# Kernel tuning notes

Measured on AMD Instinct MI355X. Metric: run time of the kernel, lower is better.

Reference implementation:

```python
import jax, jax.numpy as jnp
import numpy as np

N, D_IN, D_OUT = 8192, 256, 128

def setup_inputs() -> dict:
    key = jax.random.key(0)
    kx, kq, kk, kv = jax.random.split(key, 4)
    x = jax.random.normal(kx, (N, D_IN), dtype=jnp.float32)
    # original uses torch.rand (uniform [0,1)) for parameters
    weight_query = jax.random.uniform(kq, (D_IN, D_OUT), dtype=jnp.float32)
    weight_key = jax.random.uniform(kk, (D_IN, D_OUT), dtype=jnp.float32)
    weight_value = jax.random.uniform(kv, (D_IN, D_OUT), dtype=jnp.float32)
    return {"x": x, "weight_query": weight_query, "weight_key": weight_key, "weight_value": weight_value}

def reference(x, weight_query, weight_key, weight_value):
    queries = x @ weight_query            # [N, d_out]
    keys = x @ weight_key                 # [N, d_out]
    values = x @ weight_value             # [N, d_out]
    scale = 1.0 / jnp.sqrt(jnp.asarray(keys.shape[-1], dtype=keys.dtype))
    scores = (queries @ keys.T) * scale   # [N, N] — full score matrix, as in original
    weights = jax.nn.softmax(scores, axis=-1)
    return weights @ values               # [N, d_out]
```

## Files before the change

### kernel.cpp

```cpp
#include <hip/hip_runtime.h>
#include <math.h>


typedef float f32x4 __attribute__((ext_vector_type(4)));
typedef float f32x16 __attribute__((ext_vector_type(16)));
typedef __bf16 bf16x8 __attribute__((ext_vector_type(8)));
typedef unsigned short ushort_t;
typedef ushort_t us4 __attribute__((ext_vector_type(4)));
typedef unsigned u32x2 __attribute__((ext_vector_type(2)));

#define N_TOK 8192
#define NSPLIT 8
#define NSTEP 16

static __device__ __forceinline__ f32x16 mfma32(bf16x8 a, bf16x8 b, f32x16 c) {
  return __builtin_amdgcn_mfma_f32_32x32x16_bf16(a, b, c, 0, 0, 0);
}
static __device__ __forceinline__ void f2split(float f, ushort_t& hi, ushort_t& lo) {
  __bf16 h = (__bf16)f;
  float rem = f - (float)h;
  __bf16 l2 = (__bf16)rem;
  hi = __builtin_bit_cast(ushort_t, h);
  lo = __builtin_bit_cast(ushort_t, l2);
}
static __device__ __forceinline__ void gload16(const void* g, void* l) {
  __builtin_amdgcn_global_load_lds(
      (const __attribute__((address_space(1))) unsigned*)g,
      (__attribute__((address_space(3))) unsigned*)l, 16, 0, 0);
}
static __device__ __forceinline__ unsigned cvtpk(float lo, float hi) {
  unsigned w;
  asm("v_cvt_pk_bf16_f32 %0, %1, %2" : "=v"(w) : "v"(lo), "v"(hi));
  return w;
}

__global__ __launch_bounds__(256) void prep_kernel(
    const float* __restrict__ X, const float* __restrict__ Wq,
    const float* __restrict__ Wk, const float* __restrict__ Wv,
    ushort_t* __restrict__ Xh, ushort_t* __restrict__ Xl,
    ushort_t* __restrict__ WTh, ushort_t* __restrict__ WTl) {
  int gid = blockIdx.x * 256 + threadIdx.x;
  if (gid < 524288) {
    float4 v = reinterpret_cast<const float4*>(X)[gid];
    us4 h, l;
    ushort_t hh, ll;
    f2split(v.x, hh, ll); h[0] = hh; l[0] = ll;
    f2split(v.y, hh, ll); h[1] = hh; l[1] = ll;
    f2split(v.z, hh, ll); h[2] = hh; l[2] = ll;
    f2split(v.w, hh, ll); h[3] = hh; l[3] = ll;
    reinterpret_cast<us4*>(Xh)[gid] = h;
    reinterpret_cast<us4*>(Xl)[gid] = l;
  } else if (gid < 524288 + 98304) {
    int e = gid - 524288;
    int y = e >> 15, r = e & 32767;
    int k = r >> 7, c = r & 127;
    const float* W = (y == 0) ? Wq : (y == 1) ? Wk : Wv;
    ushort_t h, l;
    f2split(W[r], h, l);
    WTh[y * 32768 + c * 256 + k] = h;
    WTl[y * 32768 + c * 256 + k] = l;
  }
}

__global__ __launch_bounds__(256) void proj_kernel(
    const ushort_t* __restrict__ Xh, const ushort_t* __restrict__ Xl,
    const ushort_t* __restrict__ WTh, const ushort_t* __restrict__ WTl,
    ushort_t* __restrict__ Qh, ushort_t* __restrict__ Ql,
    ushort_t* __restrict__ Kh, ushort_t* __restrict__ Kl,
    ushort_t* __restrict__ VTh, ushort_t* __restrict__ VTl) {
  __shared__ __align__(16) char sm[49152];
  const int SXH = 0, SXL = 8192, SWH = 16384, SWL = 32768;
  int t = threadIdx.x, l = t & 63, wid = t >> 6;
  int c32 = l & 31, h = l >> 5;
  int wr = wid >> 1, wc = wid & 1;
  int t0 = blockIdx.x * 64, y = blockIdx.y;
  const ushort_t* WThy = WTh + y * 32768;
  const ushort_t* WTly = WTl + y * 32768;

  f32x16 zero = {};
  f32x16 acc[2];
  acc[0] = zero; acc[1] = zero;

  for (int sl = 0; sl < 4; ++sl) {
    int k0 = sl * 64;
    __syncthreads();
    #pragma unroll
    for (int j = 0; j < 12; ++j) {
      int id = wid * 12 + j;
      const ushort_t* src;
      char* dst;
      if (id < 16) {
        const ushort_t* base = (id < 8) ? Xh : Xl;
        int c_ = id & 7;
        int row = 8 * c_ + (l >> 3);
        int slot = l & 7;
        src = base + (size_t)(t0 + row) * 256 + k0 + ((slot ^ (row & 7)) * 8);
        dst = sm + ((id < 8) ? SXH : SXL) + c_ * 1024 + l * 16;
      } else {
        const ushort_t* base = (id < 32) ? WThy : WTly;
        int c_ = (id - 16) & 15;
        int row = 8 * c_ + (l >> 3);
        int slot = l & 7;
        src = base + (size_t)row * 256 + k0 + ((slot ^ (row & 7)) * 8);
        dst = sm + ((id < 32) ? SWH : SWL) + c_ * 1024 + l * 16;
      }
      gload16(src, dst);
    }
    asm volatile("s_waitcnt vmcnt(0)" ::: "memory");
    __syncthreads();
    #pragma unroll
    for (int ks = 0; ks < 4; ++ks) {
      int ar = 32 * wr + c32;
      int ao = ar * 128 + (((2 * ks + h) ^ (ar & 7)) * 16);
      bf16x8 ah = *(const bf16x8*)(sm + SXH + ao);
      bf16x8 axl = *(const bf16x8*)(sm + SXL + ao);
      #pragma unroll
      for (int ct = 0; ct < 2; ++ct) {
        int bc = 64 * wc + 32 * ct + c32;
        int bo = bc * 128 + (((2 * ks + h) ^ (bc & 7)) * 16);
        bf16x8 bh = *(const bf16x8*)(sm + SWH + bo);
        bf16x8 bl2 = *(const bf16x8*)(sm + SWL + bo);
        acc[ct] = mfma32(ah, bh, acc[ct]);
        acc[ct] = mfma32(ah, bl2, acc[ct]);
        acc[ct] = mfma32(axl, bh, acc[ct]);
      }
    }
  }

  const float QS = 0.12751744f;
  if (y < 2) {
    ushort_t* Hh = y ? Kh : Qh;
    ushort_t* Hl = y ? Kl : Ql;
    #pragma unroll
    for (int ct = 0; ct < 2; ++ct)
      #pragma unroll
      for (int r = 0; r < 16; ++r) {
        float v = acc[ct][r];
        if (y == 0) v *= QS;
        int rt = t0 + 32 * wr + (r & 3) + 8 * (r >> 2) + 4 * h;
        int cc = 64 * wc + 32 * ct + c32;
        ushort_t hh, ll;
        f2split(v, hh, ll);
        Hh[(size_t)rt * 128 + cc] = hh;
        Hl[(size_t)rt * 128 + cc] = ll;
      }
  } else {
    __syncthreads();
    #pragma unroll
    for (int ct = 0; ct < 2; ++ct)
      #pragma unroll
      for (int r = 0; r < 16; ++r) {
        float v = acc[ct][r];
        int rtl = 32 * wr + (r & 3) + 8 * (r >> 2) + 4 * h;
        int cc = 64 * wc + 32 * ct + c32;
        ushort_t hh, ll;
        f2split(v, hh, ll);
        *(ushort_t*)(sm + rtl * 272 + cc * 2) = hh;
        *(ushort_t*)(sm + 17408 + rtl * 272 + cc * 2) = ll;
      }
    __syncthreads();
    int cc = t >> 1, hs = t & 1;
    #pragma unroll
    for (int jj = 0; jj < 4; ++jj) {
      int r0 = hs * 32 + jj * 8;
      us4 a, b, a2, b2;
      #pragma unroll
      for (int e = 0; e < 4; ++e) {
        a[e]  = *(const ushort_t*)(sm + (r0 + e) * 272 + cc * 2);
        b[e]  = *(const ushort_t*)(sm + (r0 + 4 + e) * 272 + cc * 2);
        a2[e] = *(const ushort_t*)(sm + 17408 + (r0 + e) * 272 + cc * 2);
        b2[e] = *(const ushort_t*)(sm + 17408 + (r0 + 4 + e) * 272 + cc * 2);
      }
      *(us4*)(VTh + (size_t)cc * N_TOK + t0 + r0) = a;
      *(us4*)(VTh + (size_t)cc * N_TOK + t0 + r0 + 4) = b;
      *(us4*)(VTl + (size_t)cc * N_TOK + t0 + r0) = a2;
      *(us4*)(VTl + (size_t)cc * N_TOK + t0 + r0 + 4) = b2;
    }
  }
}

__global__ __launch_bounds__(256, 2) void attn_kernel(
    const ushort_t* __restrict__ Qh, const ushort_t* __restrict__ Ql,
    const ushort_t* __restrict__ Kh, const ushort_t* __restrict__ Kl,
    const ushort_t* __restrict__ VTh, const ushort_t* __restrict__ VTl,
    float* __restrict__ Op, float* __restrict__ mp, float* __restrict__ lp) {
  extern __shared__ __align__(16) char sm[];
  const int OKH = 0, OKL = 16384, OVH = 32768, OVL = 49152;
  int t = threadIdx.x, l = t & 63, wid = t >> 6;
  int c32 = l & 31, h = l >> 5;
  int bid = blockIdx.x;
  int split = bid & 7, qt = bid >> 3;
  int qb = qt * 128, kv0 = split * 1024;
  int q_lane = qb + wid * 32 + c32;

  bf16x8 qfh[8], qfl[8];
  #pragma unroll
  for (int ks = 0; ks < 8; ++ks) {
    qfh[ks] = *(const bf16x8*)(Qh + (size_t)q_lane * 128 + ks * 16 + h * 8);
    qfl[ks] = *(const bf16x8*)(Ql + (size_t)q_lane * 128 + ks * 16 + h * 8);
  }

  f32x16 zero = {};
  f32x16 od[4];
  #pragma unroll
  for (int dt = 0; dt < 4; ++dt) od[dt] = zero;
  float m = -INFINITY, lsum = 0.f;

  for (int s = 0; s < NSTEP; ++s) {
    int kb = kv0 + s * 64;
    __syncthreads();
    #pragma unroll
    for (int j = 0; j < 16; ++j) {
      int id = wid * 16 + j;
      const ushort_t* src;
      char* dst;
      if (id < 32) {
        const ushort_t* base = (id < 16) ? Kh : Kl;
        int c_ = id & 15;
        int row = 4 * c_ + (l >> 4);
        int slot = l & 15;
        src = base + (size_t)(kb + row) * 128 + ((slot ^ (row & 15)) * 8);
        dst = sm + ((id < 16) ? OKH : OKL) + c_ * 1024 + l * 16;
      } else {
        const ushort_t* base = (id < 48) ? VTh : VTl;
        int c_ = id & 15;
        int d = 8 * c_ + (l >> 3);
        int slot = l & 7;
        src = base + (size_t)d * N_TOK + kb + ((slot ^ (d & 7)) * 8);
        dst = sm + ((id < 48) ? OVH : OVL) + c_ * 1024 + l * 16;
      }
      gload16(src, dst);
    }
    asm volatile("s_waitcnt vmcnt(0)" ::: "memory");
    __syncthreads();

    f32x16 sc0 = zero, sc1 = zero;
    #pragma unroll
    for (int ks = 0; ks < 8; ++ks) {
      int so = ((2 * ks + h) ^ (c32 & 15)) * 16;
      bf16x8 a0h = *(const bf16x8*)(sm + OKH + c32 * 256 + so);
      bf16x8 a0l = *(const bf16x8*)(sm + OKL + c32 * 256 + so);
      bf16x8 a1h = *(const bf16x8*)(sm + OKH + 8192 + c32 * 256 + so);
      bf16x8 a1l = *(const bf16x8*)(sm + OKL + 8192 + c32 * 256 + so);
      sc0 = mfma32(a0h, qfh[ks], sc0);
      sc0 = mfma32(a0h, qfl[ks], sc0);
      sc0 = mfma32(a0l, qfh[ks], sc0);
      sc1 = mfma32(a1h, qfh[ks], sc1);
      sc1 = mfma32(a1h, qfl[ks], sc1);
      sc1 = mfma32(a1l, qfh[ks], sc1);
    }

    float pm = sc0[0];
    #pragma unroll
    for (int r = 1; r < 16; ++r) pm = fmaxf(pm, sc0[r]);
    #pragma unroll
    for (int r = 0; r < 16; ++r) pm = fmaxf(pm, sc1[r]);
    pm = fmaxf(pm, __shfl_xor(pm, 32));
    float mn = fmaxf(m, pm);
    float al = exp2f(m - mn);
    m = mn;
    float ps = 0.f;
    #pragma unroll
    for (int r = 0; r < 16; ++r) { sc0[r] = exp2f(sc0[r] - m); ps += sc0[r]; }
    #pragma unroll
    for (int r = 0; r < 16; ++r) { sc1[r] = exp2f(sc1[r] - m); ps += sc1[r]; }
    lsum = lsum * al + ps;
    #pragma unroll
    for (int dt = 0; dt < 4; ++dt) od[dt] *= al;

    bf16x8 pf[4];
    #pragma unroll
    for (int ks = 0; ks < 4; ++ks) {
      const f32x16& P = (ks < 2) ? sc0 : sc1;
      int r0 = 8 * (ks & 1);
      unsigned A0 = cvtpk(P[r0 + 0], P[r0 + 1]);
      unsigned A1 = cvtpk(P[r0 + 2], P[r0 + 3]);
      unsigned B0 = cvtpk(P[r0 + 4], P[r0 + 5]);
      unsigned B1 = cvtpk(P[r0 + 6], P[r0 + 7]);
      u32x2 s0 = __builtin_amdgcn_permlane32_swap(A0, B0, false, false);
      u32x2 s1 = __builtin_amdgcn_permlane32_swap(A1, B1, false, false);
      union { unsigned u[4]; bf16x8 v; } cvt;
      cvt.u[0] = s0[0]; cvt.u[1] = s1[0]; cvt.u[2] = s0[1]; cvt.u[3] = s1[1];
      pf[ks] = cvt.v;
    }

    #pragma unroll
    for (int ks = 0; ks < 4; ++ks) {
      #pragma unroll
      for (int dt = 0; dt < 4; ++dt) {
        int row = 32 * dt + c32;
        int so2 = row * 128 + (((2 * ks + h) ^ (c32 & 7)) * 16);
        bf16x8 vh = *(const bf16x8*)(sm + OVH + so2);
        bf16x8 vl2 = *(const bf16x8*)(sm + OVL + so2);
        od[dt] = mfma32(vh, pf[ks], od[dt]);
        od[dt] = mfma32(vl2, pf[ks], od[dt]);
      }
    }
  }

  lsum += __shfl_xor(lsum, 32);
  #pragma unroll
  for (int dt = 0; dt < 4; ++dt)
    #pragma unroll
    for (int r = 0; r < 16; ++r) {
      int d = 32 * dt + (r & 3) + 8 * (r >> 2) + 4 * h;
      Op[(size_t)(split * 128 + d) * N_TOK + q_lane] = od[dt][r];
    }
  if (h == 0) {
    mp[split * N_TOK + q_lane] = m;
    lp[split * N_TOK + q_lane] = lsum;
  }
}

__global__ __launch_bounds__(256) void merge_kernel(
    const float* __restrict__ Op, const float* __restrict__ mp,
    const float* __restrict__ lp, float* __restrict__ out) {
  __shared__ float accs[32][129];
  __shared__ float Ls[32];
  int t = threadIdx.x;
  int q0 = blockIdx.x * 32;
  int ql = t & 31, dr = t >> 5;
  float mm[NSPLIT], ll[NSPLIT];
  #pragma unroll
  for (int s2 = 0; s2 < NSPLIT; ++s2) {
    mm[s2] = mp[s2 * N_TOK + q0 + ql];
    ll[s2] = lp[s2 * N_TOK + q0 + ql];
  }
  float M = mm[0];
  #pragma unroll
  for (int s2 = 1; s2 < NSPLIT; ++s2) M = fmaxf(M, mm[s2]);
  float w[NSPLIT], L = 0.f;
  #pragma unroll
  for (int s2 = 0; s2 < NSPLIT; ++s2) { w[s2] = exp2f(mm[s2] - M); L += w[s2] * ll[s2]; }
  if (dr == 0) Ls[ql] = L;
  for (int dd = dr; dd < 128; dd += 8) {
    float a = 0.f;
    #pragma unroll
    for (int s2 = 0; s2 < NSPLIT; ++s2)
      a += w[s2] * Op[(size_t)(s2 * 128 + dd) * N_TOK + q0 + ql];
    accs[ql][dd] = a;
  }
  __syncthreads();
  int q = t >> 3, db = (t & 7) * 16;
  float inv = 1.0f / Ls[q];
  #pragma unroll
  for (int jj = 0; jj < 4; ++jj) {
    f32x4 v;
    #pragma unroll
    for (int e = 0; e < 4; ++e) v[e] = accs[q][db + jj * 4 + e] * inv;
    *reinterpret_cast<f32x4*>(out + (size_t)(q0 + q) * 128 + db + jj * 4) = v;
  }
}

extern "C" void kernel_launch(void* const* d_in, const int* in_sizes, int n_in,
                              void* d_out, int out_size, void* d_ws, size_t ws_size,
                              hipStream_t stream) {
  (void)in_sizes; (void)n_in; (void)out_size; (void)ws_size;
  const float* X  = (const float*)d_in[0];
  const float* Wq = (const float*)d_in[1];
  const float* Wk = (const float*)d_in[2];
  const float* Wv = (const float*)d_in[3];
  float* out = (float*)d_out;
  char* ws = (char*)d_ws;

  const size_t MB = 1048576;
  ushort_t* Qh  = (ushort_t*)(ws + 0 * MB);
  ushort_t* Ql  = (ushort_t*)(ws + 2 * MB);
  ushort_t* Kh  = (ushort_t*)(ws + 4 * MB);
  ushort_t* Kl  = (ushort_t*)(ws + 6 * MB);
  ushort_t* VTh = (ushort_t*)(ws + 8 * MB);
  ushort_t* VTl = (ushort_t*)(ws + 10 * MB);
  float* mpp = (float*)(ws + 12 * MB);
  float* lpp = (float*)(ws + 12 * MB + 262144);
  float* Op  = (float*)(ws + 12 * MB + 524288);
  ushort_t* Xh  = (ushort_t*)(ws + 12 * MB + 524288);
  ushort_t* Xl  = (ushort_t*)(ws + 16 * MB + 524288);
  ushort_t* WTh = (ushort_t*)(ws + 20 * MB + 524288);
  ushort_t* WTl = (ushort_t*)(ws + 20 * MB + 524288 + 196608);

  (void)hipFuncSetAttribute((const void*)attn_kernel,
                            hipFuncAttributeMaxDynamicSharedMemorySize, 65536);

  prep_kernel<<<2432, 256, 0, stream>>>(X, Wq, Wk, Wv, Xh, Xl, WTh, WTl);
  proj_kernel<<<dim3(128, 3), 256, 0, stream>>>(Xh, Xl, WTh, WTl,
                                                Qh, Ql, Kh, Kl, VTh, VTl);
  attn_kernel<<<512, 256, 65536, stream>>>(Qh, Ql, Kh, Kl, VTh, VTl, Op, mpp, lpp);
  merge_kernel<<<256, 256, 0, stream>>>(Op, mpp, lpp, out);
}
```

Baseline: 168.4 us.

## Double-buffer 32-token KV tiles with async prefetch and lazy softmax rescale

Restructures the attention inner loop to process 32-key tiles instead of 64, double-buffered in LDS so the next tile's K/V global-to-LDS loads overlap the current tile's MFMA and softmax work. Each wave now issues a fixed set of precomputed load offsets for one of the four streams (Kh, Kl, VTh, VTl). It also adds a lazy max rescale that only updates m and rescales the accumulators when the new max exceeds the old by more than 8, and sets wave priority around the MFMA blocks. The trade-offs are twice as many loop iterations with an extra barrier each, plus a redundant wraparound prefetch on the last step.

```diff
diff --git a/kernel.cpp b/kernel.cpp
--- a/kernel.cpp
+++ b/kernel.cpp
@@ -11,7 +11,8 @@
 
 #define N_TOK 8192
 #define NSPLIT 8
-#define NSTEP 16
+#define KVB 32
+#define NSTEP2 32
 
 static __device__ __forceinline__ f32x16 mfma32(bf16x8 a, bf16x8 b, f32x16 c) {
   return __builtin_amdgcn_mfma_f32_32x32x16_bf16(a, b, c, 0, 0, 0);
@@ -185,7 +186,6 @@
     const ushort_t* __restrict__ VTh, const ushort_t* __restrict__ VTl,
     float* __restrict__ Op, float* __restrict__ mp, float* __restrict__ lp) {
   extern __shared__ __align__(16) char sm[];
-  const int OKH = 0, OKL = 16384, OVH = 32768, OVL = 49152;
   int t = threadIdx.x, l = t & 63, wid = t >> 6;
   int c32 = l & 31, h = l >> 5;
   int bid = blockIdx.x;
@@ -200,83 +200,92 @@
     qfl[ks] = *(const bf16x8*)(Ql + (size_t)q_lane * 128 + ks * 16 + h * 8);
   }
 
+  const ushort_t* gbase;
+  int stepstride;
+  int offs[8];
+  if (wid < 2) {
+    gbase = ((wid == 0) ? Kh : Kl) + (size_t)kv0 * 128;
+    stepstride = KVB * 128;
+    #pragma unroll
+    for (int j = 0; j < 8; ++j) {
+      int row = 4 * j + (l >> 4);
+      offs[j] = row * 128 + (((l & 15) ^ (row & 15)) * 8);
+    }
+  } else {
+    gbase = ((wid == 2) ? VTh : VTl) + kv0;
+    stepstride = KVB;
+    #pragma unroll
+    for (int j = 0; j < 8; ++j) {
+      int d = 16 * j + (l >> 2);
+      offs[j] = d * N_TOK + (((l & 3) ^ ((l >> 2) & 3)) * 8);
+    }
+  }
+  char* ldsbase = sm + wid * 8192 + l * 16;
+
   f32x16 zero = {};
   f32x16 od[4];
   #pragma unroll
   for (int dt = 0; dt < 4; ++dt) od[dt] = zero;
   float m = -INFINITY, lsum = 0.f;
 
-  for (int s = 0; s < NSTEP; ++s) {
-    int kb = kv0 + s * 64;
-    __syncthreads();
-    #pragma unroll
-    for (int j = 0; j < 16; ++j) {
-      int id = wid * 16 + j;
-      const ushort_t* src;
-      char* dst;
-      if (id < 32) {
-        const ushort_t* base = (id < 16) ? Kh : Kl;
-        int c_ = id & 15;
-        int row = 4 * c_ + (l >> 4);
-        int slot = l & 15;
-        src = base + (size_t)(kb + row) * 128 + ((slot ^ (row & 15)) * 8);
-        dst = sm + ((id < 16) ? OKH : OKL) + c_ * 1024 + l * 16;
-      } else {
-        const ushort_t* base = (id < 48) ? VTh : VTl;
-        int c_ = id & 15;
-        int d = 8 * c_ + (l >> 3);
-        int slot = l & 7;
-        src = base + (size_t)d * N_TOK + kb + ((slot ^ (d & 7)) * 8);
-        dst = sm + ((id < 48) ? OVH : OVL) + c_ * 1024 + l * 16;
-      }
-      gload16(src, dst);
-    }
-    asm volatile("s_waitcnt vmcnt(0)" ::: "memory");
-    __syncthreads();
-
-    f32x16 sc0 = zero, sc1 = zero;
+  {
+    const ushort_t* sb = gbase;
+    #pragma unroll
+    for (int j = 0; j < 8; ++j) gload16(sb + offs[j], ldsbase + j * 1024);
+  }
+
+  for (int s = 0; s < NSTEP2; ++s) {
+    int cur = s & 1;
+    {
+      const ushort_t* sb = gbase + (size_t)((s + 1) & (NSTEP2 - 1)) * stepstride;
+      char* db = ldsbase + (cur ^ 1) * 32768;
+      #pragma unroll
+      for (int j = 0; j < 8; ++j) gload16(sb + offs[j], db + j * 1024);
+    }
+    asm volatile("s_waitcnt vmcnt(8)" ::: "memory");
+    __syncthreads();
+
+    const char* bK = sm + cur * 32768;
+    const char* bV = bK + 16384;
+
+    f32x16 sc = zero;
+    __builtin_amdgcn_s_setprio(1);
     #pragma unroll
     for (int ks = 0; ks < 8; ++ks) {
       int so = ((2 * ks + h) ^ (c32 & 15)) * 16;
-      bf16x8 a0h = *(const bf16x8*)(sm + OKH + c32 * 256 + so);
-      bf16x8 a0l = *(const bf16x8*)(sm + OKL + c32 * 256 + so);
-      bf16x8 a1h = *(const bf16x8*)(sm + OKH + 8192 + c32 * 256 + so);
-      bf16x8 a1l = *(const bf16x8*)(sm + OKL + 8192 + c32 * 256 + so);
-      sc0 = mfma32(a0h, qfh[ks], sc0);
-      sc0 = mfma32(a0h, qfl[ks], sc0);
-      sc0 = mfma32(a0l, qfh[ks], sc0);
-      sc1 = mfma32(a1h, qfh[ks], sc1);
-      sc1 = mfma32(a1h, qfl[ks], sc1);
-      sc1 = mfma32(a1l, qfh[ks], sc1);
-    }
-
-    float pm = sc0[0];
-    #pragma unroll
-    for (int r = 1; r < 16; ++r) pm = fmaxf(pm, sc0[r]);
-    #pragma unroll
-    for (int r = 0; r < 16; ++r) pm = fmaxf(pm, sc1[r]);
+      bf16x8 ah = *(const bf16x8*)(bK + c32 * 256 + so);
+      bf16x8 al2 = *(const bf16x8*)(bK + 8192 + c32 * 256 + so);
+      sc = mfma32(ah, qfh[ks], sc);
+      sc = mfma32(ah, qfl[ks], sc);
+      sc = mfma32(al2, qfh[ks], sc);
+    }
+    __builtin_amdgcn_s_setprio(0);
+
+    float pm = sc[0];
+    #pragma unroll
+    for (int r = 1; r < 16; ++r) pm = fmaxf(pm, sc[r]);
     pm = fmaxf(pm, __shfl_xor(pm, 32));
-    float mn = fmaxf(m, pm);
-    float al = exp2f(m - mn);
-    m = mn;
+    if (!__all(pm <= m + 8.0f)) {
+      float mn = fmaxf(m, pm);
+      float al = exp2f(m - mn);
+      m = mn;
+      lsum *= al;
+      #pragma unroll
+      for (int dt = 0; dt < 4; ++dt) od[dt] *= al;
+    }
     float ps = 0.f;
     #pragma unroll
-    for (int r = 0; r < 16; ++r) { sc0[r] = exp2f(sc0[r] - m); ps += sc0[r]; }
-    #pragma unroll
-    for (int r = 0; r < 16; ++r) { sc1[r] = exp2f(sc1[r] - m); ps += sc1[r]; }
-    lsum = lsum * al + ps;
-    #pragma unroll
-    for (int dt = 0; dt < 4; ++dt) od[dt] *= al;
-
-    bf16x8 pf[4];
-    #pragma unroll
-    for (int ks = 0; ks < 4; ++ks) {
-      const f32x16& P = (ks < 2) ? sc0 : sc1;
-      int r0 = 8 * (ks & 1);
-      unsigned A0 = cvtpk(P[r0 + 0], P[r0 + 1]);
-      unsigned A1 = cvtpk(P[r0 + 2], P[r0 + 3]);
-      unsigned B0 = cvtpk(P[r0 + 4], P[r0 + 5]);
-      unsigned B1 = cvtpk(P[r0 + 6], P[r0 + 7]);
+    for (int r = 0; r < 16; ++r) { sc[r] = exp2f(sc[r] - m); ps += sc[r]; }
+    lsum += ps;
+
+    bf16x8 pf[2];
+    #pragma unroll
+    for (int ks = 0; ks < 2; ++ks) {
+      int r0 = 8 * ks;
+      unsigned A0 = cvtpk(sc[r0 + 0], sc[r0 + 1]);
+      unsigned A1 = cvtpk(sc[r0 + 2], sc[r0 + 3]);
+      unsigned B0 = cvtpk(sc[r0 + 4], sc[r0 + 5]);
+      unsigned B1 = cvtpk(sc[r0 + 6], sc[r0 + 7]);
       u32x2 s0 = __builtin_amdgcn_permlane32_swap(A0, B0, false, false);
       u32x2 s1 = __builtin_amdgcn_permlane32_swap(A1, B1, false, false);
       union { unsigned u[4]; bf16x8 v; } cvt;
@@ -284,18 +293,21 @@
       pf[ks] = cvt.v;
     }
 
-    #pragma unroll
-    for (int ks = 0; ks < 4; ++ks) {
+    __builtin_amdgcn_s_setprio(1);
+    #pragma unroll
+    for (int ks = 0; ks < 2; ++ks) {
       #pragma unroll
       for (int dt = 0; dt < 4; ++dt) {
         int row = 32 * dt + c32;
-        int so2 = row * 128 + (((2 * ks + h) ^ (c32 & 7)) * 16);
-        bf16x8 vh = *(const bf16x8*)(sm + OVH + so2);
-        bf16x8 vl2 = *(const bf16x8*)(sm + OVL + so2);
+        int so2 = row * 64 + (((2 * ks + h) ^ (row & 3)) * 16);
+        bf16x8 vh = *(const bf16x8*)(bV + so2);
+        bf16x8 vl2 = *(const bf16x8*)(bV + 8192 + so2);
         od[dt] = mfma32(vh, pf[ks], od[dt]);
         od[dt] = mfma32(vl2, pf[ks], od[dt]);
       }
     }
+    __builtin_amdgcn_s_setprio(0);
+    __syncthreads();
   }
 
   lsum += __shfl_xor(lsum, 32);
```

Measured after the change: 174.4 us. 3.6% more time.
